# Performance work log

Measured on AMD Instinct MI355X. Metric: run time of the kernel, lower is better.

The kernel has to match this reference:

```python
import jax, jax.numpy as jnp
import numpy as np

B, N = 32, 64
ATTR, STATE, REL, GDIM = 4, 8, 4, 32
NF = 128

def _ln(x, w, b, eps=1e-5):
    mu = jnp.mean(x, axis=-1, keepdims=True)
    var = jnp.mean((x - mu) ** 2, axis=-1, keepdims=True)
    return (x - mu) * jax.lax.rsqrt(var + eps) * w + b

def setup_inputs() -> dict:
    key = jax.random.key(0)
    ks = iter(jax.random.split(key, 32))
    d = {}
    d['attrs'] = jax.random.normal(next(ks), (B, N, ATTR), jnp.float32)
    d['states'] = jax.random.normal(next(ks), (B, N, STATE), jnp.float32)
    d['actions'] = jnp.zeros((B, N, 4), jnp.float32)  # action=False, unused
    d['rel_attrs'] = jax.random.normal(next(ks), (B, N, N, REL), jnp.float32)
    def w(shape):
        return jax.random.normal(next(ks), shape, jnp.float32) * 0.05
    d['oe_w0'] = w((NF, ATTR + STATE)); d['oe_b0'] = jnp.zeros((NF,), jnp.float32)
    d['oe_w1'] = w((NF, NF));            d['oe_b1'] = jnp.zeros((NF,), jnp.float32)
    d['re_w0'] = w((NF, STATE + REL + 2 * ATTR)); d['re_b0'] = jnp.zeros((NF,), jnp.float32)
    d['re_w1'] = w((NF, NF));            d['re_b1'] = jnp.zeros((NF,), jnp.float32)
    d['rp_w'] = w((NF, NF + 2 * NF));    d['rp_b'] = jnp.zeros((NF,), jnp.float32)
    d['rp_lnw'] = jnp.ones((NF,), jnp.float32); d['rp_lnb'] = jnp.zeros((NF,), jnp.float32)
    d['pp_w'] = w((NF, 2 * NF));         d['pp_b'] = jnp.zeros((NF,), jnp.float32)
    d['pp_lnw'] = jnp.ones((NF,), jnp.float32); d['pp_lnb'] = jnp.zeros((NF,), jnp.float32)
    d['pr_w0'] = w((NF, NF));            d['pr_b0'] = jnp.zeros((NF,), jnp.float32)
    d['pr_w1'] = w((GDIM, NF));          d['pr_b1'] = jnp.zeros((GDIM,), jnp.float32)
    d['pstep'] = 2
    return d

def reference(attrs, states, actions, rel_attrs,
              oe_w0, oe_b0, oe_w1, oe_b1,
              re_w0, re_b0, re_w1, re_b1,
              rp_w, rp_b, rp_lnw, rp_lnb,
              pp_w, pp_b, pp_lnw, pp_lnb,
              pr_w0, pr_b0, pr_w1, pr_b1, pstep):
    lin = lambda x, w, b: jnp.einsum('...i,oi->...o', x, w) + b
    # ---- encode nodes: [B,N,attr+state] -> [B,N,NF] (action=False) ----
    obj_in = jnp.concatenate([attrs, states], axis=2)
    obj_encode = jax.nn.relu(lin(jax.nn.relu(lin(obj_in, oe_w0, oe_b0)), oe_w1, oe_b1))
    # ---- encode edges over dense N x N pairs ----
    rel_states = states[:, :, None, :] - states[:, None, :, :]        # B,N,N,state
    recv_attr = jnp.broadcast_to(attrs[:, :, None, :], (attrs.shape[0], attrs.shape[1], attrs.shape[1], attrs.shape[2]))
    send_attr = jnp.broadcast_to(attrs[:, None, :, :], recv_attr.shape)
    rel_in = jnp.concatenate([rel_attrs, rel_states, recv_attr, send_attr], axis=3)
    rel_encode = jax.nn.relu(lin(jax.nn.relu(lin(rel_in, re_w0, re_b0)), re_w1, re_b1))  # B,N,N,NF
    # ---- propagation steps ----
    for _ in range(pstep):
        sh = rel_encode.shape[:3] + (obj_encode.shape[-1],)
        recv = jnp.broadcast_to(obj_encode[:, :, None, :], sh)
        send = jnp.broadcast_to(obj_encode[:, None, :, :], sh)
        rel_effect = jax.nn.relu(_ln(lin(jnp.concatenate([rel_encode, recv, send], axis=3), rp_w, rp_b), rp_lnw, rp_lnb))
        rel_agg = rel_effect.sum(axis=2)                               # B,N,NF
        obj_encode = jax.nn.relu(_ln(lin(jnp.concatenate([obj_encode, rel_agg], axis=2), pp_w, pp_b), pp_lnw, pp_lnb))
    # ---- predict + tanh (state_encoder has tanh=True) ----
    out = lin(jax.nn.relu(lin(obj_encode, pr_w0, pr_b0)), pr_w1, pr_b1)
    return jnp.tanh(out)
```

## Files before the change

kernel.cpp:

```cpp
#include <hip/hip_runtime.h>
#include <hip/hip_bf16.h>


#define ROWS 2048
typedef unsigned short u16;
typedef unsigned int u32;
typedef __attribute__((ext_vector_type(8))) short bf16x8;
typedef __attribute__((ext_vector_type(4))) float f32x4;

__device__ __forceinline__ float bsu(u16 u) { return __uint_as_float(((u32)u) << 16); }
__device__ __forceinline__ u16 f2b(float f) {
    u32 u = __float_as_uint(f);
    u32 r = (u + 0x7fffu + ((u >> 16) & 1u)) >> 16;
    return (u16)r;
}
__device__ __forceinline__ u32 pk2(float a, float b) {
    __hip_bfloat162 h = __float22bfloat162_rn(float2{a, b});
    union { __hip_bfloat162 h; u32 u; } c; c.h = h; return c.u;
}
__device__ __forceinline__ bf16x8 ldcvt8(const float* __restrict__ p) {
    float4 a = *(const float4*)p;
    float4 b = *(const float4*)(p + 4);
    union { u32 u[4]; bf16x8 v; } x;
    x.u[0] = pk2(a.x, a.y); x.u[1] = pk2(a.z, a.w);
    x.u[2] = pk2(b.x, b.y); x.u[3] = pk2(b.z, b.w);
    return x.v;
}

__global__ __launch_bounds__(256)
void k_node(const float* __restrict__ attrs, const float* __restrict__ states,
            const float* __restrict__ oe_w0, const float* __restrict__ oe_b0,
            const float* __restrict__ oe_w1, const float* __restrict__ oe_b1,
            const float* __restrict__ re_w0, const float* __restrict__ re_b0,
            const float* __restrict__ rp_w,  const float* __restrict__ rp_b,
            const float* __restrict__ re_w1, const float* __restrict__ pp_w,
            const float* __restrict__ pr_w0, const float* __restrict__ pr_w1,
            u16* __restrict__ re_w1b, u16* __restrict__ web, u16* __restrict__ pp_wb,
            u16* __restrict__ wrecvb, u16* __restrict__ wsendb,
            u16* __restrict__ pr_w0b, u16* __restrict__ pr_w1b,
            u16* __restrict__ objb, float* __restrict__ nr, float* __restrict__ ns,
            float* __restrict__ recvT, float* __restrict__ sendT)
{
    const int r0 = blockIdx.x * 16;
    const int t = threadIdx.x;
    __shared__ float xs[16][12];
    __shared__ float w0s[1536];
    __shared__ float rw0s[2560];
    __shared__ __align__(16) u16 hb[16 * 136];
    __shared__ __align__(16) u16 ob[16 * 136];

    {
        int gid = blockIdx.x * 256 + t;
        for (int i = gid; i < 118784; i += 32768) {
            int idx = i;
            if (idx < 16384) { re_w1b[idx] = f2b(re_w1[idx]); continue; }
            idx -= 16384;
            if (idx < 16384) { web[idx] = f2b(rp_w[(idx >> 7) * 384 + (idx & 127)]); continue; }
            idx -= 16384;
            if (idx < 32768) { pp_wb[idx] = f2b(pp_w[idx]); continue; }
            idx -= 32768;
            if (idx < 16384) { wrecvb[idx] = f2b(rp_w[(idx >> 7) * 384 + 128 + (idx & 127)]); continue; }
            idx -= 16384;
            if (idx < 16384) { wsendb[idx] = f2b(rp_w[(idx >> 7) * 384 + 256 + (idx & 127)]); continue; }
            idx -= 16384;
            if (idx < 16384) { pr_w0b[idx] = f2b(pr_w0[idx]); continue; }
            idx -= 16384;
            pr_w1b[idx] = f2b(pr_w1[idx]);
        }
    }

    if (t < 192) { int row = t / 12, c = t - row * 12;
        xs[row][c] = (c < 4) ? attrs[(r0 + row) * 4 + c] : states[(r0 + row) * 8 + (c - 4)]; }
    for (int i = t; i < 1536; i += 256) w0s[i] = oe_w0[i];
    for (int i = t; i < 2560; i += 256) rw0s[i] = re_w0[i];
    __syncthreads();

    for (int e = t; e < 2048; e += 256) {
        int row = e >> 7, o = e & 127;
        float h = oe_b0[o];
#pragma unroll
        for (int k = 0; k < 12; k++) h += w0s[o * 12 + k] * xs[row][k];
        hb[row * 136 + o] = f2b(fmaxf(h, 0.f));
        float s0 = 0.f, a0 = 0.f, a1 = 0.f;
#pragma unroll
        for (int k = 0; k < 8; k++) s0 += rw0s[o * 20 + 4 + k] * xs[row][4 + k];
#pragma unroll
        for (int k = 0; k < 4; k++) {
            a0 += rw0s[o * 20 + 12 + k] * xs[row][k];
            a1 += rw0s[o * 20 + 16 + k] * xs[row][k];
        }
        nr[(r0 + row) * 128 + o] = s0 + a0 + re_b0[o];
        ns[(r0 + row) * 128 + o] = a1 - s0;
    }
    __syncthreads();

    const int wave = t >> 6, lane = t & 63, tx = lane & 15, quad = lane >> 4;

    bf16x8 afr[4];
#pragma unroll
    for (int kk = 0; kk < 4; kk++) afr[kk] = *(const bf16x8*)&hb[tx * 136 + kk * 32 + quad * 8];
    f32x4 acc[2]; acc[0] = (f32x4){0.f,0.f,0.f,0.f}; acc[1] = acc[0];
#pragma unroll
    for (int ot = 0; ot < 2; ot++) {
        int o = (wave * 2 + ot) * 16 + tx;
#pragma unroll
        for (int kk = 0; kk < 4; kk++) {
            bf16x8 bfr = ldcvt8(&oe_w1[o * 128 + kk * 32 + quad * 8]);
            acc[ot] = __builtin_amdgcn_mfma_f32_16x16x32_bf16(afr[kk], bfr, acc[ot], 0, 0, 0);
        }
    }
#pragma unroll
    for (int ot = 0; ot < 2; ot++) {
        int o = (wave * 2 + ot) * 16 + tx;
        float bia = oe_b1[o];
#pragma unroll
        for (int r = 0; r < 4; r++)
            ob[(quad * 4 + r) * 136 + o] = f2b(fmaxf(acc[ot][r] + bia, 0.f));
    }
    __syncthreads();
    { int m = t >> 4, c = t & 15;
      *(uint4*)&objb[(r0 + m) * 128 + c * 8] = *(const uint4*)&ob[m * 136 + c * 8]; }

#pragma unroll
    for (int kk = 0; kk < 4; kk++) afr[kk] = *(const bf16x8*)&ob[tx * 136 + kk * 32 + quad * 8];
    f32x4 ar[2], an[2];
    ar[0] = (f32x4){0.f,0.f,0.f,0.f}; ar[1] = ar[0]; an[0] = ar[0]; an[1] = ar[0];
#pragma unroll
    for (int ot = 0; ot < 2; ot++) {
        int o = (wave * 2 + ot) * 16 + tx;
#pragma unroll
        for (int kk = 0; kk < 4; kk++) {
            bf16x8 br = ldcvt8(&rp_w[o * 384 + 128 + kk * 32 + quad * 8]);
            ar[ot] = __builtin_amdgcn_mfma_f32_16x16x32_bf16(afr[kk], br, ar[ot], 0, 0, 0);
            bf16x8 bs = ldcvt8(&rp_w[o * 384 + 256 + kk * 32 + quad * 8]);
            an[ot] = __builtin_amdgcn_mfma_f32_16x16x32_bf16(afr[kk], bs, an[ot], 0, 0, 0);
        }
    }
#pragma unroll
    for (int ot = 0; ot < 2; ot++) {
        int o = (wave * 2 + ot) * 16 + tx;
        float rb = rp_b[o];
#pragma unroll
        for (int r = 0; r < 4; r++) {
            recvT[(r0 + quad * 4 + r) * 128 + o] = ar[ot][r] + rb;
            sendT[(r0 + quad * 4 + r) * 128 + o] = an[ot][r];
        }
    }
}

__global__ __launch_bounds__(256)
void k_edge_fused(const float* __restrict__ rel_attrs,
                  const float* __restrict__ re_w0, const u16* __restrict__ re_w1b,
                  const u16* __restrict__ web, const float* __restrict__ re_b1,
                  const float* __restrict__ rp_lnw, const float* __restrict__ rp_lnb,
                  const float* __restrict__ nr, const float* __restrict__ ns,
                  const float* __restrict__ recvT, const float* __restrict__ sendT,
                  u16* __restrict__ Ebuf, u16* __restrict__ aggb)
{
    const int blkg = blockIdx.x;
    const int b = blkg >> 6;
    const int t = threadIdx.x;
    __shared__ __align__(16) u16 hsb[64 * 144];
    __shared__ float lnws[128], lnbs[128];
    __shared__ float redS[256], redQ[256];

    if (t < 128) { lnws[t] = rp_lnw[t]; lnbs[t] = rp_lnb[t]; }

    {
        const int o0 = (t & 15) * 8;
        const int jb = t >> 4;
        float4 nr0 = *(const float4*)&nr[blkg * 128 + o0];
        float4 nr1 = *(const float4*)&nr[blkg * 128 + o0 + 4];
        float4 wreg[8];
#pragma unroll
        for (int k = 0; k < 8; k++) wreg[k] = *(const float4*)&re_w0[(o0 + k) * 20];
#pragma unroll
        for (int it = 0; it < 4; it++) {
            int j = jb + it * 16;
            float4 ra = *(const float4*)&rel_attrs[((size_t)blkg * 64 + j) * 4];
            const float* nsp = &ns[(b * 64 + j) * 128 + o0];
            float4 na = *(const float4*)nsp;
            float4 nb = *(const float4*)(nsp + 4);
            float v[8];
            v[0] = nr0.x + na.x; v[1] = nr0.y + na.y; v[2] = nr0.z + na.z; v[3] = nr0.w + na.w;
            v[4] = nr1.x + nb.x; v[5] = nr1.y + nb.y; v[6] = nr1.z + nb.z; v[7] = nr1.w + nb.w;
#pragma unroll
            for (int k = 0; k < 8; k++) {
                v[k] += wreg[k].x * ra.x + wreg[k].y * ra.y + wreg[k].z * ra.z + wreg[k].w * ra.w;
                v[k] = fmaxf(v[k], 0.f);
            }
            union { u32 u[4]; uint4 q; } p;
            p.u[0] = pk2(v[0], v[1]); p.u[1] = pk2(v[2], v[3]);
            p.u[2] = pk2(v[4], v[5]); p.u[3] = pk2(v[6], v[7]);
            *(uint4*)&hsb[j * 144 + o0] = p.q;
        }
    }

    const int w = t >> 6, lane = t & 63, tx = lane & 15, quad = lane >> 4;
    const int ob = w * 32;

    bf16x8 b1[2][4];
#pragma unroll
    for (int ot = 0; ot < 2; ot++)
#pragma unroll
        for (int kk = 0; kk < 4; kk++)
            b1[ot][kk] = *(const bf16x8*)&re_w1b[(ob + ot * 16 + tx) * 128 + kk * 32 + quad * 8];
    __syncthreads();

    f32x4 acc[4][2];
#pragma unroll
    for (int jt = 0; jt < 4; jt++) { acc[jt][0] = (f32x4){0.f,0.f,0.f,0.f}; acc[jt][1] = acc[jt][0]; }
#pragma unroll
    for (int jt = 0; jt < 4; jt++) {
        bf16x8 afr[4];
#pragma unroll
        for (int kk = 0; kk < 4; kk++)
            afr[kk] = *(const bf16x8*)&hsb[(jt * 16 + tx) * 144 + kk * 32 + quad * 8];
#pragma unroll
        for (int ot = 0; ot < 2; ot++)
#pragma unroll
            for (int kk = 0; kk < 4; kk++)
                acc[jt][ot] = __builtin_amdgcn_mfma_f32_16x16x32_bf16(afr[kk], b1[ot][kk], acc[jt][ot], 0, 0, 0);
    }
    __syncthreads();

    {
        float bia0 = re_b1[ob + tx], bia1 = re_b1[ob + 16 + tx];
#pragma unroll
        for (int jt = 0; jt < 4; jt++)
#pragma unroll
            for (int r = 0; r < 4; r++) {
                int j = jt * 16 + quad * 4 + r;
                hsb[j * 144 + ob + tx]      = f2b(fmaxf(acc[jt][0][r] + bia0, 0.f));
                hsb[j * 144 + ob + 16 + tx] = f2b(fmaxf(acc[jt][1][r] + bia1, 0.f));
            }
    }
    bf16x8 b2[2][4];
#pragma unroll
    for (int ot = 0; ot < 2; ot++)
#pragma unroll
        for (int kk = 0; kk < 4; kk++)
            b2[ot][kk] = *(const bf16x8*)&web[(ob + ot * 16 + tx) * 128 + kk * 32 + quad * 8];
    __syncthreads();

    f32x4 acc2[4][2];
#pragma unroll
    for (int jt = 0; jt < 4; jt++) { acc2[jt][0] = (f32x4){0.f,0.f,0.f,0.f}; acc2[jt][1] = acc2[jt][0]; }
#pragma unroll
    for (int jt = 0; jt < 4; jt++) {
        bf16x8 afr[4];
#pragma unroll
        for (int kk = 0; kk < 4; kk++)
            afr[kk] = *(const bf16x8*)&hsb[(jt * 16 + tx) * 144 + kk * 32 + quad * 8];
#pragma unroll
        for (int ot = 0; ot < 2; ot++)
#pragma unroll
            for (int kk = 0; kk < 4; kk++)
                acc2[jt][ot] = __builtin_amdgcn_mfma_f32_16x16x32_bf16(afr[kk], b2[ot][kk], acc2[jt][ot], 0, 0, 0);
    }

#pragma unroll
    for (int jt = 0; jt < 4; jt++)
#pragma unroll
        for (int ot = 0; ot < 2; ot++) {
            uint2 ev;
            ev.x = pk2(acc2[jt][ot][0], acc2[jt][ot][1]);
            ev.y = pk2(acc2[jt][ot][2], acc2[jt][ot][3]);
            *(uint2*)(Ebuf + ((size_t)((blkg * 4 + jt) * 8 + (2 * w + ot)) * 64 + lane) * 4) = ev;
        }

    {
        float rv0 = recvT[blkg * 128 + ob + tx];
        float rv1 = recvT[blkg * 128 + ob + 16 + tx];
#pragma unroll
        for (int jt = 0; jt < 4; jt++)
#pragma unroll
            for (int r = 0; r < 4; r++) {
                int j = b * 64 + jt * 16 + quad * 4 + r;
                acc2[jt][0][r] += rv0 + sendT[j * 128 + ob + tx];
                acc2[jt][1][r] += rv1 + sendT[j * 128 + ob + 16 + tx];
            }
    }

#pragma unroll
    for (int jt = 0; jt < 4; jt++) {
        float s4[4], q4[4];
#pragma unroll
        for (int r = 0; r < 4; r++) {
            float a0 = acc2[jt][0][r], a1 = acc2[jt][1][r];
            s4[r] = a0 + a1; q4[r] = a0 * a0 + a1 * a1;
        }
#pragma unroll
        for (int m = 1; m < 16; m <<= 1)
#pragma unroll
            for (int r = 0; r < 4; r++) {
                s4[r] += __shfl_xor(s4[r], m, 64);
                q4[r] += __shfl_xor(q4[r], m, 64);
            }
        if (tx == 0)
#pragma unroll
            for (int r = 0; r < 4; r++) {
                redS[w * 64 + jt * 16 + quad * 4 + r] = s4[r];
                redQ[w * 64 + jt * 16 + quad * 4 + r] = q4[r];
            }
    }
    __syncthreads();

    {
        float lw0 = lnws[ob + tx], lb0 = lnbs[ob + tx];
        float lw1 = lnws[ob + 16 + tx], lb1 = lnbs[ob + 16 + tx];
        float ag0 = 0.f, ag1 = 0.f;
#pragma unroll
        for (int jt = 0; jt < 4; jt++)
#pragma unroll
            for (int r = 0; r < 4; r++) {
                int row = jt * 16 + quad * 4 + r;
                float ss = redS[row] + redS[64 + row] + redS[128 + row] + redS[192 + row];
                float qq = redQ[row] + redQ[64 + row] + redQ[128 + row] + redQ[192 + row];
                float mu = ss * (1.f / 128.f);
                float rsd = rsqrtf(qq * (1.f / 128.f) - mu * mu + 1e-5f);
                float z0 = (acc2[jt][0][r] - mu) * rsd * lw0 + lb0;
                float z1 = (acc2[jt][1][r] - mu) * rsd * lw1 + lb1;
                ag0 += fmaxf(z0, 0.f);
                ag1 += fmaxf(z1, 0.f);
            }
        ag0 += __shfl_xor(ag0, 16, 64); ag0 += __shfl_xor(ag0, 32, 64);
        ag1 += __shfl_xor(ag1, 16, 64); ag1 += __shfl_xor(ag1, 32, 64);
        if (quad == 0) {
            aggb[blkg * 128 + ob + tx]      = f2b(ag0);
            aggb[blkg * 128 + ob + 16 + tx] = f2b(ag1);
        }
    }
}

__global__ __launch_bounds__(256)
void k_prop_edge2(const u16* __restrict__ Ebuf,
                  const float* __restrict__ rp_lnw, const float* __restrict__ rp_lnb,
                  const float* __restrict__ recvT, const float* __restrict__ sendT,
                  u16* __restrict__ aggb)
{
    const int blk = blockIdx.x;
    const int b = blk >> 6;
    const int t = threadIdx.x;
    __shared__ float scr[16 * 132];
    __shared__ float lnws[128], lnbs[128];
    if (t < 128) { lnws[t] = rp_lnw[t]; lnbs[t] = rp_lnb[t]; }
    __syncthreads();

    const int wave = t >> 6, lane = t & 63, tx = lane & 15, quad = lane >> 4;
    const int tid = blk * 4 + wave;
    const int jrow = wave * 16 + quad * 4;

    float y[8][4];
#pragma unroll
    for (int oo = 0; oo < 8; oo++) {
        uint2 ev = *(const uint2*)(Ebuf + ((size_t)(tid * 8 + oo) * 64 + lane) * 4);
        const int o = oo * 16 + tx;
        float rv = recvT[blk * 128 + o];
        float e0 = bsu((u16)(ev.x & 0xffff)), e1 = bsu((u16)(ev.x >> 16));
        float e2 = bsu((u16)(ev.y & 0xffff)), e3 = bsu((u16)(ev.y >> 16));
        y[oo][0] = e0 + rv + sendT[(b * 64 + jrow + 0) * 128 + o];
        y[oo][1] = e1 + rv + sendT[(b * 64 + jrow + 1) * 128 + o];
        y[oo][2] = e2 + rv + sendT[(b * 64 + jrow + 2) * 128 + o];
        y[oo][3] = e3 + rv + sendT[(b * 64 + jrow + 3) * 128 + o];
    }
    float s[4], q[4];
#pragma unroll
    for (int r = 0; r < 4; r++) {
        s[r] = 0.f; q[r] = 0.f;
#pragma unroll
        for (int oo = 0; oo < 8; oo++) { s[r] += y[oo][r]; q[r] += y[oo][r] * y[oo][r]; }
    }
#pragma unroll
    for (int m = 1; m < 16; m <<= 1) {
#pragma unroll
        for (int r = 0; r < 4; r++) {
            s[r] += __shfl_xor(s[r], m, 64);
            q[r] += __shfl_xor(q[r], m, 64);
        }
    }
    float mu[4], rs[4];
#pragma unroll
    for (int r = 0; r < 4; r++) {
        mu[r] = s[r] * (1.f / 128.f);
        rs[r] = rsqrtf(q[r] * (1.f / 128.f) - mu[r] * mu[r] + 1e-5f);
    }
    float pa[8];
#pragma unroll
    for (int oo = 0; oo < 8; oo++) {
        const int o = oo * 16 + tx;
        float lw = lnws[o], lb = lnbs[o];
        float p = 0.f;
#pragma unroll
        for (int r = 0; r < 4; r++) {
            float z = (y[oo][r] - mu[r]) * rs[r] * lw + lb;
            p += fmaxf(z, 0.f);
        }
        pa[oo] = p;
    }
    const int grp = wave * 4 + quad;
#pragma unroll
    for (int oo = 0; oo < 8; oo++) scr[grp * 132 + oo * 16 + tx] = pa[oo];
    __syncthreads();
    if (t < 128) {
        float sum = 0.f;
#pragma unroll
        for (int gg = 0; gg < 16; gg++) sum += scr[gg * 132 + t];
        aggb[blk * 128 + t] = f2b(sum);
    }
}

__global__ __launch_bounds__(256)
void k_pn0(const u16* __restrict__ aggb,
           const u16* __restrict__ pp_wb, const float* __restrict__ pp_b,
           const float* __restrict__ pp_lnw, const float* __restrict__ pp_lnb,
           const u16* __restrict__ wrecvb, const u16* __restrict__ wsendb,
           const float* __restrict__ rp_b,
           u16* __restrict__ objb, float* __restrict__ recvT, float* __restrict__ sendT)
{
    const int r0 = blockIdx.x * 16;
    const int t = threadIdx.x;
    __shared__ __align__(16) u16 ab[16 * 264];
    __shared__ __align__(16) u16 ob[16 * 136];
    __shared__ float redS[64], redQ[64];

    for (int i = t; i < 512; i += 256) {
        int m = i >> 5, c = i & 31;
        uint4 v = (c < 16) ? *(const uint4*)&objb[(r0 + m) * 128 + (c & 15) * 8]
                           : *(const uint4*)&aggb[(r0 + m) * 128 + (c - 16) * 8];
        *(uint4*)&ab[m * 264 + c * 8] = v;
    }
    __syncthreads();

    const int wave = t >> 6, lane = t & 63, tx = lane & 15, quad = lane >> 4;
    bf16x8 afr[8];
#pragma unroll
    for (int kk = 0; kk < 8; kk++) afr[kk] = *(const bf16x8*)&ab[tx * 264 + kk * 32 + quad * 8];
    f32x4 acc[2]; acc[0] = (f32x4){0.f,0.f,0.f,0.f}; acc[1] = acc[0];
#pragma unroll
    for (int ot = 0; ot < 2; ot++) {
        int o = (wave * 2 + ot) * 16 + tx;
#pragma unroll
        for (int kk = 0; kk < 8; kk++) {
            bf16x8 bfr = *(const bf16x8*)&pp_wb[o * 256 + kk * 32 + quad * 8];
            acc[ot] = __builtin_amdgcn_mfma_f32_16x16x32_bf16(afr[kk], bfr, acc[ot], 0, 0, 0);
        }
    }
#pragma unroll
    for (int ot = 0; ot < 2; ot++) {
        float bia = pp_b[(wave * 2 + ot) * 16 + tx];
#pragma unroll
        for (int r = 0; r < 4; r++) acc[ot][r] += bia;
    }

    float s[4], q[4];
#pragma unroll
    for (int r = 0; r < 4; r++) {
        s[r] = acc[0][r] + acc[1][r];
        q[r] = acc[0][r] * acc[0][r] + acc[1][r] * acc[1][r];
    }
#pragma unroll
    for (int m = 1; m < 16; m <<= 1) {
#pragma unroll
        for (int r = 0; r < 4; r++) {
            s[r] += __shfl_xor(s[r], m, 64);
            q[r] += __shfl_xor(q[r], m, 64);
        }
    }
    if (tx == 0) {
#pragma unroll
        for (int r = 0; r < 4; r++) {
            redS[wave * 16 + quad * 4 + r] = s[r];
            redQ[wave * 16 + quad * 4 + r] = q[r];
        }
    }
    __syncthreads();
    float mu[4], rs[4];
#pragma unroll
    for (int r = 0; r < 4; r++) {
        int m = quad * 4 + r;
        float ss = redS[m] + redS[16 + m] + redS[32 + m] + redS[48 + m];
        float qq = redQ[m] + redQ[16 + m] + redQ[32 + m] + redQ[48 + m];
        mu[r] = ss * (1.f / 128.f);
        rs[r] = rsqrtf(qq * (1.f / 128.f) - mu[r] * mu[r] + 1e-5f);
    }
#pragma unroll
    for (int ot = 0; ot < 2; ot++) {
        int o = (wave * 2 + ot) * 16 + tx;
        float lw = pp_lnw[o], lb = pp_lnb[o];
#pragma unroll
        for (int r = 0; r < 4; r++) {
            float z = (acc[ot][r] - mu[r]) * rs[r] * lw + lb;
            ob[(quad * 4 + r) * 136 + o] = f2b(fmaxf(z, 0.f));
        }
    }
    __syncthreads();
    { int m = t >> 4, c = t & 15;
      *(uint4*)&objb[(r0 + m) * 128 + c * 8] = *(const uint4*)&ob[m * 136 + c * 8]; }

    bf16x8 af2[4];
#pragma unroll
    for (int kk = 0; kk < 4; kk++) af2[kk] = *(const bf16x8*)&ob[tx * 136 + kk * 32 + quad * 8];
    f32x4 ar[2], an[2];
    ar[0] = (f32x4){0.f,0.f,0.f,0.f}; ar[1] = ar[0]; an[0] = ar[0]; an[1] = ar[0];
#pragma unroll
    for (int ot = 0; ot < 2; ot++) {
        int o = (wave * 2 + ot) * 16 + tx;
#pragma unroll
        for (int kk = 0; kk < 4; kk++) {
            bf16x8 br = *(const bf16x8*)&wrecvb[o * 128 + kk * 32 + quad * 8];
            ar[ot] = __builtin_amdgcn_mfma_f32_16x16x32_bf16(af2[kk], br, ar[ot], 0, 0, 0);
            bf16x8 bs = *(const bf16x8*)&wsendb[o * 128 + kk * 32 + quad * 8];
            an[ot] = __builtin_amdgcn_mfma_f32_16x16x32_bf16(af2[kk], bs, an[ot], 0, 0, 0);
        }
    }
#pragma unroll
    for (int ot = 0; ot < 2; ot++) {
        int o = (wave * 2 + ot) * 16 + tx;
        float rb = rp_b[o];
#pragma unroll
        for (int r = 0; r < 4; r++) {
            recvT[(r0 + quad * 4 + r) * 128 + o] = ar[ot][r] + rb;
            sendT[(r0 + quad * 4 + r) * 128 + o] = an[ot][r];
        }
    }
}

__global__ __launch_bounds__(256)
void k_pn1pred(const u16* __restrict__ aggb,
               const u16* __restrict__ pp_wb, const float* __restrict__ pp_b,
               const float* __restrict__ pp_lnw, const float* __restrict__ pp_lnb,
               const u16* __restrict__ objb,
               const u16* __restrict__ pr_w0b, const float* __restrict__ pr_b0,
               const u16* __restrict__ pr_w1b, const float* __restrict__ pr_b1,
               float* __restrict__ out)
{
    const int r0 = blockIdx.x * 16;
    const int t = threadIdx.x;
    __shared__ __align__(16) u16 ab[16 * 264];
    __shared__ __align__(16) u16 ob[16 * 136];
    __shared__ __align__(16) u16 hb2[16 * 136];
    __shared__ float redS[64], redQ[64];

    for (int i = t; i < 512; i += 256) {
        int m = i >> 5, c = i & 31;
        uint4 v = (c < 16) ? *(const uint4*)&objb[(r0 + m) * 128 + (c & 15) * 8]
                           : *(const uint4*)&aggb[(r0 + m) * 128 + (c - 16) * 8];
        *(uint4*)&ab[m * 264 + c * 8] = v;
    }
    __syncthreads();

    const int wave = t >> 6, lane = t & 63, tx = lane & 15, quad = lane >> 4;
    bf16x8 afr[8];
#pragma unroll
    for (int kk = 0; kk < 8; kk++) afr[kk] = *(const bf16x8*)&ab[tx * 264 + kk * 32 + quad * 8];
    f32x4 acc[2]; acc[0] = (f32x4){0.f,0.f,0.f,0.f}; acc[1] = acc[0];
#pragma unroll
    for (int ot = 0; ot < 2; ot++) {
        int o = (wave * 2 + ot) * 16 + tx;
#pragma unroll
        for (int kk = 0; kk < 8; kk++) {
            bf16x8 bfr = *(const bf16x8*)&pp_wb[o * 256 + kk * 32 + quad * 8];
            acc[ot] = __builtin_amdgcn_mfma_f32_16x16x32_bf16(afr[kk], bfr, acc[ot], 0, 0, 0);
        }
    }
#pragma unroll
    for (int ot = 0; ot < 2; ot++) {
        float bia = pp_b[(wave * 2 + ot) * 16 + tx];
#pragma unroll
        for (int r = 0; r < 4; r++) acc[ot][r] += bia;
    }

    float s[4], q[4];
#pragma unroll
    for (int r = 0; r < 4; r++) {
        s[r] = acc[0][r] + acc[1][r];
        q[r] = acc[0][r] * acc[0][r] + acc[1][r] * acc[1][r];
    }
#pragma unroll
    for (int m = 1; m < 16; m <<= 1) {
#pragma unroll
        for (int r = 0; r < 4; r++) {
            s[r] += __shfl_xor(s[r], m, 64);
            q[r] += __shfl_xor(q[r], m, 64);
        }
    }
    if (tx == 0) {
#pragma unroll
        for (int r = 0; r < 4; r++) {
            redS[wave * 16 + quad * 4 + r] = s[r];
            redQ[wave * 16 + quad * 4 + r] = q[r];
        }
    }
    __syncthreads();
    float mu[4], rs[4];
#pragma unroll
    for (int r = 0; r < 4; r++) {
        int m = quad * 4 + r;
        float ss = redS[m] + redS[16 + m] + redS[32 + m] + redS[48 + m];
        float qq = redQ[m] + redQ[16 + m] + redQ[32 + m] + redQ[48 + m];
        mu[r] = ss * (1.f / 128.f);
        rs[r] = rsqrtf(qq * (1.f / 128.f) - mu[r] * mu[r] + 1e-5f);
    }
#pragma unroll
    for (int ot = 0; ot < 2; ot++) {
        int o = (wave * 2 + ot) * 16 + tx;
        float lw = pp_lnw[o], lb = pp_lnb[o];
#pragma unroll
        for (int r = 0; r < 4; r++) {
            float z = (acc[ot][r] - mu[r]) * rs[r] * lw + lb;
            ob[(quad * 4 + r) * 136 + o] = f2b(fmaxf(z, 0.f));
        }
    }
    __syncthreads();

    bf16x8 af2[4];
#pragma unroll
    for (int kk = 0; kk < 4; kk++) af2[kk] = *(const bf16x8*)&ob[tx * 136 + kk * 32 + quad * 8];
    f32x4 ah[2]; ah[0] = (f32x4){0.f,0.f,0.f,0.f}; ah[1] = ah[0];
#pragma unroll
    for (int ot = 0; ot < 2; ot++) {
        int o = (wave * 2 + ot) * 16 + tx;
#pragma unroll
        for (int kk = 0; kk < 4; kk++) {
            bf16x8 bfr = *(const bf16x8*)&pr_w0b[o * 128 + kk * 32 + quad * 8];
            ah[ot] = __builtin_amdgcn_mfma_f32_16x16x32_bf16(af2[kk], bfr, ah[ot], 0, 0, 0);
        }
    }
#pragma unroll
    for (int ot = 0; ot < 2; ot++) {
        int o = (wave * 2 + ot) * 16 + tx;
        float bia = pr_b0[o];
#pragma unroll
        for (int r = 0; r < 4; r++)
            hb2[(quad * 4 + r) * 136 + o] = f2b(fmaxf(ah[ot][r] + bia, 0.f));
    }
    __syncthreads();

    if (wave < 2) {
        bf16x8 af3[4];
#pragma unroll
        for (int kk = 0; kk < 4; kk++) af3[kk] = *(const bf16x8*)&hb2[tx * 136 + kk * 32 + quad * 8];
        f32x4 a2 = (f32x4){0.f,0.f,0.f,0.f};
        int o = wave * 16 + tx;
#pragma unroll
        for (int kk = 0; kk < 4; kk++) {
            bf16x8 bfr = *(const bf16x8*)&pr_w1b[o * 128 + kk * 32 + quad * 8];
            a2 = __builtin_amdgcn_mfma_f32_16x16x32_bf16(af3[kk], bfr, a2, 0, 0, 0);
        }
        float bia = pr_b1[o];
#pragma unroll
        for (int r = 0; r < 4; r++)
            out[(r0 + quad * 4 + r) * 32 + o] = tanhf(a2[r] + bia);
    }
}

extern "C" void kernel_launch(void* const* d_in, const int* in_sizes, int n_in,
                              void* d_out, int out_size, void* d_ws, size_t ws_size,
                              hipStream_t stream)
{
    const float* attrs    = (const float*)d_in[0];
    const float* states   = (const float*)d_in[1];
    const float* rel_attrs= (const float*)d_in[3];
    const float* oe_w0 = (const float*)d_in[4];
    const float* oe_b0 = (const float*)d_in[5];
    const float* oe_w1 = (const float*)d_in[6];
    const float* oe_b1 = (const float*)d_in[7];
    const float* re_w0 = (const float*)d_in[8];
    const float* re_b0 = (const float*)d_in[9];
    const float* re_w1 = (const float*)d_in[10];
    const float* re_b1 = (const float*)d_in[11];
    const float* rp_w  = (const float*)d_in[12];
    const float* rp_b  = (const float*)d_in[13];
    const float* rp_lnw= (const float*)d_in[14];
    const float* rp_lnb= (const float*)d_in[15];
    const float* pp_w  = (const float*)d_in[16];
    const float* pp_b  = (const float*)d_in[17];
    const float* pp_lnw= (const float*)d_in[18];
    const float* pp_lnb= (const float*)d_in[19];
    const float* pr_w0 = (const float*)d_in[20];
    const float* pr_b0 = (const float*)d_in[21];
    const float* pr_w1 = (const float*)d_in[22];
    const float* pr_b1 = (const float*)d_in[23];

    float* ws    = (float*)d_ws;
    float* nr    = ws;
    float* ns    = nr    + ROWS * 128;
    float* recvT = ns    + ROWS * 128;
    float* sendT = recvT + ROWS * 128;
    u16* re_w1b = (u16*)(sendT + ROWS * 128);
    u16* web    = re_w1b + 16384;
    u16* pp_wb  = web    + 16384;
    u16* wrecvb = pp_wb  + 32768;
    u16* wsendb = wrecvb + 16384;
    u16* pr_w0b = wsendb + 16384;
    u16* pr_w1b = pr_w0b + 16384;
    u16* objb   = pr_w1b + 4096;
    u16* aggb   = objb + ROWS * 128;
    u16* Ebuf   = aggb + ROWS * 128;

    k_node<<<128, 256, 0, stream>>>(attrs, states, oe_w0, oe_b0, oe_w1, oe_b1,
                                    re_w0, re_b0, rp_w, rp_b,
                                    re_w1, pp_w, pr_w0, pr_w1,
                                    re_w1b, web, pp_wb, wrecvb, wsendb, pr_w0b, pr_w1b,
                                    objb, nr, ns, recvT, sendT);
    k_edge_fused<<<2048, 256, 0, stream>>>(rel_attrs, re_w0, re_w1b, web, re_b1,
                                           rp_lnw, rp_lnb, nr, ns, recvT, sendT,
                                           Ebuf, aggb);
    k_pn0<<<128, 256, 0, stream>>>(aggb, pp_wb, pp_b, pp_lnw, pp_lnb,
                                   wrecvb, wsendb, rp_b, objb, recvT, sendT);
    k_prop_edge2<<<2048, 256, 0, stream>>>(Ebuf, rp_lnw, rp_lnb, recvT, sendT, aggb);
    k_pn1pred<<<128, 256, 0, stream>>>(aggb, pp_wb, pp_b, pp_lnw, pp_lnb, objb,
                                       pr_w0b, pr_b0, pr_w1b, pr_b1, (float*)d_out);
}
```

Before: 190.1 us.

## Compute LayerNorm mean via precomputed weight column sums instead of row reductions

The LayerNorm mean over output features is split by linearity into three parts: the edge term is computed with an extra MFMA against the column-sum of the bf16 weights, and the receiver and sender terms are computed once per node in the node kernels. Each part is stored in its own small buffer. This removes the sum shuffle-reductions and the redS shared array from both edge kernels, leaving only the sum-of-squares reduction. In exchange it adds MFMAs, extra global buffers and synchronisations in the node kernels, and bf16 rounding of the summed weights may change the numerics of the mean slightly.

```diff
diff --git a/kernel.cpp b/kernel.cpp
--- a/kernel.cpp
+++ b/kernel.cpp
@@ -37,9 +37,10 @@
             const float* __restrict__ pr_w0, const float* __restrict__ pr_w1,
             u16* __restrict__ re_w1b, u16* __restrict__ web, u16* __restrict__ pp_wb,
             u16* __restrict__ wrecvb, u16* __restrict__ wsendb,
-            u16* __restrict__ pr_w0b, u16* __restrict__ pr_w1b,
+            u16* __restrict__ pr_w0b, u16* __restrict__ pr_w1b, u16* __restrict__ wsumb,
             u16* __restrict__ objb, float* __restrict__ nr, float* __restrict__ ns,
-            float* __restrict__ recvT, float* __restrict__ sendT)
+            float* __restrict__ recvT, float* __restrict__ sendT,
+            float* __restrict__ recvS0, float* __restrict__ sendS0)
 {
     const int r0 = blockIdx.x * 16;
     const int t = threadIdx.x;
@@ -68,6 +69,11 @@
             pr_w1b[idx] = f2b(pr_w1[idx]);
         }
     }
+    if (blockIdx.x == 0 && t < 128) {
+        float s = 0.f;
+        for (int o = 0; o < 128; o++) s += bsu(f2b(rp_w[o * 384 + t]));
+        wsumb[t] = f2b(s);
+    }
 
     if (t < 192) { int row = t / 12, c = t - row * 12;
         xs[row][c] = (c < 4) ? attrs[(r0 + row) * 4 + c] : states[(r0 + row) * 8 + (c - 4)]; }
@@ -136,33 +142,54 @@
             an[ot] = __builtin_amdgcn_mfma_f32_16x16x32_bf16(afr[kk], bs, an[ot], 0, 0, 0);
         }
     }
-#pragma unroll
-    for (int ot = 0; ot < 2; ot++) {
-        int o = (wave * 2 + ot) * 16 + tx;
-        float rb = rp_b[o];
-#pragma unroll
-        for (int r = 0; r < 4; r++) {
-            recvT[(r0 + quad * 4 + r) * 128 + o] = ar[ot][r] + rb;
+    float rbv[2] = { rp_b[(wave * 2 + 0) * 16 + tx], rp_b[(wave * 2 + 1) * 16 + tx] };
+#pragma unroll
+    for (int ot = 0; ot < 2; ot++) {
+        int o = (wave * 2 + ot) * 16 + tx;
+#pragma unroll
+        for (int r = 0; r < 4; r++) {
+            recvT[(r0 + quad * 4 + r) * 128 + o] = ar[ot][r] + rbv[ot];
             sendT[(r0 + quad * 4 + r) * 128 + o] = an[ot][r];
         }
+    }
+    __syncthreads();
+    float* fr  = (float*)hb;
+    float* fs2 = (float*)ob;
+#pragma unroll
+    for (int r = 0; r < 4; r++) {
+        int row = quad * 4 + r;
+        fr[row * 68 + wave * 16 + tx]  = (ar[0][r] + rbv[0]) + (ar[1][r] + rbv[1]);
+        fs2[row * 68 + wave * 16 + tx] = an[0][r] + an[1][r];
+    }
+    __syncthreads();
+    if (t < 32) {
+        int p = t >> 4, row = t & 15;
+        const float* src = p ? fs2 : fr;
+        float s = 0.f;
+#pragma unroll
+        for (int k = 0; k < 64; k++) s += src[row * 68 + k];
+        (p ? sendS0 : recvS0)[r0 + row] = s;
     }
 }
 
 __global__ __launch_bounds__(256)
 void k_edge_fused(const float* __restrict__ rel_attrs,
                   const float* __restrict__ re_w0, const u16* __restrict__ re_w1b,
-                  const u16* __restrict__ web, const float* __restrict__ re_b1,
+                  const u16* __restrict__ web, const u16* __restrict__ wsumb,
+                  const float* __restrict__ re_b1,
                   const float* __restrict__ rp_lnw, const float* __restrict__ rp_lnb,
                   const float* __restrict__ nr, const float* __restrict__ ns,
                   const float* __restrict__ recvT, const float* __restrict__ sendT,
-                  u16* __restrict__ Ebuf, u16* __restrict__ aggb)
+                  const float* __restrict__ recvS0, const float* __restrict__ sendS0,
+                  u16* __restrict__ Ebuf, float* __restrict__ rowsumE,
+                  u16* __restrict__ aggb)
 {
     const int blkg = blockIdx.x;
     const int b = blkg >> 6;
     const int t = threadIdx.x;
     __shared__ __align__(16) u16 hsb[64 * 144];
     __shared__ float lnws[128], lnbs[128];
-    __shared__ float redS[256], redQ[256];
+    __shared__ float redQ[256];
 
     if (t < 128) { lnws[t] = rp_lnw[t]; lnbs[t] = rp_lnb[t]; }
 
@@ -241,11 +268,18 @@
 #pragma unroll
         for (int kk = 0; kk < 4; kk++)
             b2[ot][kk] = *(const bf16x8*)&web[(ob + ot * 16 + tx) * 128 + kk * 32 + quad * 8];
-    __syncthreads();
-
-    f32x4 acc2[4][2];
-#pragma unroll
-    for (int jt = 0; jt < 4; jt++) { acc2[jt][0] = (f32x4){0.f,0.f,0.f,0.f}; acc2[jt][1] = acc2[jt][0]; }
+    bf16x8 bws[4];
+#pragma unroll
+    for (int kk = 0; kk < 4; kk++)
+        bws[kk] = *(const bf16x8*)&wsumb[kk * 32 + quad * 8];
+    __syncthreads();
+
+    f32x4 acc2[4][2], acc_ws[4];
+#pragma unroll
+    for (int jt = 0; jt < 4; jt++) {
+        acc2[jt][0] = (f32x4){0.f,0.f,0.f,0.f}; acc2[jt][1] = acc2[jt][0];
+        acc_ws[jt] = acc2[jt][0];
+    }
 #pragma unroll
     for (int jt = 0; jt < 4; jt++) {
         bf16x8 afr[4];
@@ -257,6 +291,9 @@
 #pragma unroll
             for (int kk = 0; kk < 4; kk++)
                 acc2[jt][ot] = __builtin_amdgcn_mfma_f32_16x16x32_bf16(afr[kk], b2[ot][kk], acc2[jt][ot], 0, 0, 0);
+#pragma unroll
+        for (int kk = 0; kk < 4; kk++)
+            acc_ws[jt] = __builtin_amdgcn_mfma_f32_16x16x32_bf16(afr[kk], bws[kk], acc_ws[jt], 0, 0, 0);
     }
 
 #pragma unroll
@@ -268,6 +305,11 @@
             ev.y = pk2(acc2[jt][ot][2], acc2[jt][ot][3]);
             *(uint2*)(Ebuf + ((size_t)((blkg * 4 + jt) * 8 + (2 * w + ot)) * 64 + lane) * 4) = ev;
         }
+    if (w == 0 && tx == 0) {
+#pragma unroll
+        for (int jt = 0; jt < 4; jt++)
+            *(f32x4*)&rowsumE[(size_t)blkg * 64 + jt * 16 + quad * 4] = acc_ws[jt];
+    }
 
     {
         float rv0 = recvT[blkg * 128 + ob + tx];
@@ -284,46 +326,42 @@
 
 #pragma unroll
     for (int jt = 0; jt < 4; jt++) {
-        float s4[4], q4[4];
+        float q4[4];
 #pragma unroll
         for (int r = 0; r < 4; r++) {
             float a0 = acc2[jt][0][r], a1 = acc2[jt][1][r];
-            s4[r] = a0 + a1; q4[r] = a0 * a0 + a1 * a1;
+            q4[r] = a0 * a0 + a1 * a1;
         }
 #pragma unroll
         for (int m = 1; m < 16; m <<= 1)
 #pragma unroll
-            for (int r = 0; r < 4; r++) {
-                s4[r] += __shfl_xor(s4[r], m, 64);
-                q4[r] += __shfl_xor(q4[r], m, 64);
-            }
+            for (int r = 0; r < 4; r++) q4[r] += __shfl_xor(q4[r], m, 64);
         if (tx == 0)
 #pragma unroll
-            for (int r = 0; r < 4; r++) {
-                redS[w * 64 + jt * 16 + quad * 4 + r] = s4[r];
-                redQ[w * 64 + jt * 16 + quad * 4 + r] = q4[r];
-            }
+            for (int r = 0; r < 4; r++) redQ[w * 64 + jt * 16 + quad * 4 + r] = q4[r];
     }
     __syncthreads();
 
     {
+        float recvSi = recvS0[blkg];
         float lw0 = lnws[ob + tx], lb0 = lnbs[ob + tx];
         float lw1 = lnws[ob + 16 + tx], lb1 = lnbs[ob + 16 + tx];
         float ag0 = 0.f, ag1 = 0.f;
 #pragma unroll
-        for (int jt = 0; jt < 4; jt++)
+        for (int jt = 0; jt < 4; jt++) {
+            f32x4 ssf = *(const f32x4*)&sendS0[b * 64 + jt * 16 + quad * 4];
 #pragma unroll
             for (int r = 0; r < 4; r++) {
                 int row = jt * 16 + quad * 4 + r;
-                float ss = redS[row] + redS[64 + row] + redS[128 + row] + redS[192 + row];
                 float qq = redQ[row] + redQ[64 + row] + redQ[128 + row] + redQ[192 + row];
-                float mu = ss * (1.f / 128.f);
+                float mu = (acc_ws[jt][r] + recvSi + ssf[r]) * (1.f / 128.f);
                 float rsd = rsqrtf(qq * (1.f / 128.f) - mu * mu + 1e-5f);
                 float z0 = (acc2[jt][0][r] - mu) * rsd * lw0 + lb0;
                 float z1 = (acc2[jt][1][r] - mu) * rsd * lw1 + lb1;
                 ag0 += fmaxf(z0, 0.f);
                 ag1 += fmaxf(z1, 0.f);
             }
+        }
         ag0 += __shfl_xor(ag0, 16, 64); ag0 += __shfl_xor(ag0, 32, 64);
         ag1 += __shfl_xor(ag1, 16, 64); ag1 += __shfl_xor(ag1, 32, 64);
         if (quad == 0) {
@@ -334,9 +372,10 @@
 }
 
 __global__ __launch_bounds__(256)
-void k_prop_edge2(const u16* __restrict__ Ebuf,
+void k_prop_edge2(const u16* __restrict__ Ebuf, const float* __restrict__ rowsumE,
                   const float* __restrict__ rp_lnw, const float* __restrict__ rp_lnb,
                   const float* __restrict__ recvT, const float* __restrict__ sendT,
+                  const float* __restrict__ recvS1, const float* __restrict__ sendS1,
                   u16* __restrict__ aggb)
 {
     const int blk = blockIdx.x;
@@ -364,25 +403,25 @@
         y[oo][2] = e2 + rv + sendT[(b * 64 + jrow + 2) * 128 + o];
         y[oo][3] = e3 + rv + sendT[(b * 64 + jrow + 3) * 128 + o];
     }
-    float s[4], q[4];
+    float q[4];
 #pragma unroll
     for (int r = 0; r < 4; r++) {
-        s[r] = 0.f; q[r] = 0.f;
-#pragma unroll
-        for (int oo = 0; oo < 8; oo++) { s[r] += y[oo][r]; q[r] += y[oo][r] * y[oo][r]; }
-    }
-#pragma unroll
-    for (int m = 1; m < 16; m <<= 1) {
-#pragma unroll
-        for (int r = 0; r < 4; r++) {
-            s[r] += __shfl_xor(s[r], m, 64);
-            q[r] += __shfl_xor(q[r], m, 64);
-        }
-    }
+        q[r] = 0.f;
+#pragma unroll
+        for (int oo = 0; oo < 8; oo++) q[r] += y[oo][r] * y[oo][r];
+    }
+#pragma unroll
+    for (int m = 1; m < 16; m <<= 1)
+#pragma unroll
+        for (int r = 0; r < 4; r++) q[r] += __shfl_xor(q[r], m, 64);
+
+    float recvSi = recvS1[blk];
+    f32x4 rse = *(const f32x4*)&rowsumE[(size_t)blk * 64 + jrow];
+    f32x4 ssf = *(const f32x4*)&sendS1[b * 64 + jrow];
     float mu[4], rs[4];
 #pragma unroll
     for (int r = 0; r < 4; r++) {
-        mu[r] = s[r] * (1.f / 128.f);
+        mu[r] = (rse[r] + recvSi + ssf[r]) * (1.f / 128.f);
         rs[r] = rsqrtf(q[r] * (1.f / 128.f) - mu[r] * mu[r] + 1e-5f);
     }
     float pa[8];
@@ -416,7 +455,8 @@
            const float* __restrict__ pp_lnw, const float* __restrict__ pp_lnb,
            const u16* __restrict__ wrecvb, const u16* __restrict__ wsendb,
            const float* __restrict__ rp_b,
-           u16* __restrict__ objb, float* __restrict__ recvT, float* __restrict__ sendT)
+           u16* __restrict__ objb, float* __restrict__ recvT, float* __restrict__ sendT,
+           float* __restrict__ recvS1, float* __restrict__ sendS1)
 {
     const int r0 = blockIdx.x * 16;
     const int t = threadIdx.x;
@@ -514,15 +554,33 @@
             an[ot] = __builtin_amdgcn_mfma_f32_16x16x32_bf16(af2[kk], bs, an[ot], 0, 0, 0);
         }
     }
-#pragma unroll
-    for (int ot = 0; ot < 2; ot++) {
-        int o = (wave * 2 + ot) * 16 + tx;
-        float rb = rp_b[o];
-#pragma unroll
-        for (int r = 0; r < 4; r++) {
-            recvT[(r0 + quad * 4 + r) * 128 + o] = ar[ot][r] + rb;
+    float rbv[2] = { rp_b[(wave * 2 + 0) * 16 + tx], rp_b[(wave * 2 + 1) * 16 + tx] };
+#pragma unroll
+    for (int ot = 0; ot < 2; ot++) {
+        int o = (wave * 2 + ot) * 16 + tx;
+#pragma unroll
+        for (int r = 0; r < 4; r++) {
+            recvT[(r0 + quad * 4 + r) * 128 + o] = ar[ot][r] + rbv[ot];
             sendT[(r0 + quad * 4 + r) * 128 + o] = an[ot][r];
         }
+    }
+    __syncthreads();
+    float* fr  = (float*)ab;
+    float* fs2 = ((float*)ab) + 1056;
+#pragma unroll
+    for (int r = 0; r < 4; r++) {
+        int row = quad * 4 + r;
+        fr[row * 66 + wave * 16 + tx]  = (ar[0][r] + rbv[0]) + (ar[1][r] + rbv[1]);
+        fs2[row * 66 + wave * 16 + tx] = an[0][r] + an[1][r];
+    }
+    __syncthreads();
+    if (t < 32) {
+        int p = t >> 4, row = t & 15;
+        const float* src = p ? fs2 : fr;
+        float s2 = 0.f;
+#pragma unroll
+        for (int k = 0; k < 64; k++) s2 += src[row * 66 + k];
+        (p ? sendS1 : recvS1)[r0 + row] = s2;
     }
 }
 
@@ -636,7 +694,6 @@
             hb2[(quad * 4 + r) * 136 + o] = f2b(fmaxf(ah[ot][r] + bia, 0.f));
     }
     __syncthreads();
-
     if (wave < 2) {
         bf16x8 af3[4];
 #pragma unroll
@@ -683,12 +740,18 @@
     const float* pr_w1 = (const float*)d_in[22];
     const float* pr_b1 = (const float*)d_in[23];
 
-    float* ws    = (float*)d_ws;
-    float* nr    = ws;
-    float* ns    = nr    + ROWS * 128;
-    float* recvT = ns    + ROWS * 128;
-    float* sendT = recvT + ROWS * 128;
-    u16* re_w1b = (u16*)(sendT + ROWS * 128);
+    float* ws     = (float*)d_ws;
+    float* nr     = ws;
+    float* ns     = nr    + ROWS * 128;
+    float* recvT  = ns    + ROWS * 128;
+    float* sendT  = recvT + ROWS * 128;
+    float* recvS0 = sendT + ROWS * 128;
+    float* sendS0 = recvS0 + ROWS;
+    float* recvS1 = sendS0 + ROWS;
+    float* sendS1 = recvS1 + ROWS;
+    float* rowsumE= sendS1 + ROWS;
+    u16* wsumb  = (u16*)(rowsumE + ROWS * 64);
+    u16* re_w1b = wsumb + 128;
     u16* web    = re_w1b + 16384;
     u16* pp_wb  = web    + 16384;
     u16* wrecvb = pp_wb  + 32768;
@@ -702,14 +765,16 @@
     k_node<<<128, 256, 0, stream>>>(attrs, states, oe_w0, oe_b0, oe_w1, oe_b1,
                                     re_w0, re_b0, rp_w, rp_b,
                                     re_w1, pp_w, pr_w0, pr_w1,
-                                    re_w1b, web, pp_wb, wrecvb, wsendb, pr_w0b, pr_w1b,
-                                    objb, nr, ns, recvT, sendT);
-    k_edge_fused<<<2048, 256, 0, stream>>>(rel_attrs, re_w0, re_w1b, web, re_b1,
+                                    re_w1b, web, pp_wb, wrecvb, wsendb, pr_w0b, pr_w1b, wsumb,
+                                    objb, nr, ns, recvT, sendT, recvS0, sendS0);
+    k_edge_fused<<<2048, 256, 0, stream>>>(rel_attrs, re_w0, re_w1b, web, wsumb, re_b1,
                                            rp_lnw, rp_lnb, nr, ns, recvT, sendT,
-                                           Ebuf, aggb);
+                                           recvS0, sendS0, Ebuf, rowsumE, aggb);
     k_pn0<<<128, 256, 0, stream>>>(aggb, pp_wb, pp_b, pp_lnw, pp_lnb,
-                                   wrecvb, wsendb, rp_b, objb, recvT, sendT);
-    k_prop_edge2<<<2048, 256, 0, stream>>>(Ebuf, rp_lnw, rp_lnb, recvT, sendT, aggb);
+                                   wrecvb, wsendb, rp_b, objb, recvT, sendT,
+                                   recvS1, sendS1);
+    k_prop_edge2<<<2048, 256, 0, stream>>>(Ebuf, rowsumE, rp_lnw, rp_lnb,
+                                           recvT, sendT, recvS1, sendS1, aggb);
     k_pn1pred<<<128, 256, 0, stream>>>(aggb, pp_wb, pp_b, pp_lnw, pp_lnb, objb,
                                        pr_w0b, pr_b0, pr_w1b, pr_b1, (float*)d_out);
 }
```

New measurement: 191.1 us. Within noise of the previous version (+0.5%).
